# Kernel tuning notes

Hardware: AMD Instinct MI355X
Metric: run time of the kernel (lower is better)

The kernel has to match this reference:

```python
import jax, jax.numpy as jnp
import numpy as np

T = 524288
AABB = 4.0
BETA_MIN = 0.1
L_ENC = 4
NL = np.array([16, 22, 30, 42, 58, 80, 111, 154, 213, 295, 407, 563, 777, 1074, 1483, 2048])
# corner offsets, same ordering as the torch code's vertices[:,0..7]
OFFS = np.array([[0,0,0],[1,0,0],[0,1,0],[1,1,0],[0,0,1],[1,0,1],[0,1,1],[1,1,1]])
PRIMES = np.array([1, 2654435761, 805459861], dtype=np.uint32)


def hash_features(xn, tables):
    # xn: [N,3] normalized positions in hash-grid space; tables: [16, T, 2]
    Ns = jnp.asarray(NL, jnp.float32)                      # [16]
    xs = xn[:, None, :] * Ns[None, :, None]                # [N,16,3]
    fl = jnp.floor(xs)
    loc = xs - fl                                          # trilinear weights input
    fli = fl.astype(jnp.int32).astype(jnp.uint32)          # wraparound == int32 bit pattern
    offs = jnp.asarray(OFFS, jnp.uint32)                   # [8,3]
    pr = jnp.asarray(PRIMES, jnp.uint32)
    # spatial hash per corner, per level (avoid materializing [N,16,8,3] vertices)
    a = (fli[:, :, None, 0] + offs[None, None, :, 0]) * pr[0]
    b = (fli[:, :, None, 1] + offs[None, None, :, 1]) * pr[1]
    c = (fli[:, :, None, 2] + offs[None, None, :, 2]) * pr[2]
    h = ((a ^ b) ^ c) % jnp.uint32(T)                      # [N,16,8]
    lvl_off = (jnp.arange(len(NL), dtype=jnp.uint32) * jnp.uint32(T))[None, :, None]
    flat_idx = (h + lvl_off).astype(jnp.int32)             # index into flattened tables
    feats = tables.reshape(-1, tables.shape[-1])[flat_idx] # [N,16,8,2] gather
    offf = jnp.asarray(OFFS, jnp.float32)
    lp = loc[:, :, None, :]
    w = jnp.prod(lp * offf + (1.0 - lp) * (1.0 - offf), axis=-1)  # [N,16,8]
    out = jnp.einsum('nlc,nlcf->nlf', w, feats)            # trilinear interp
    return out.reshape(out.shape[0], -1)                   # [N, 16*2], level-major


def pos_enc(d):
    parts = [d]
    for j in range(L_ENC):
        parts.append(jnp.sin((2.0 ** j) * d))
        parts.append(jnp.cos((2.0 ** j) * d))
    return jnp.concatenate(parts, axis=1)                  # [N,27]


def _forward(x, d, appearance_idx, transient_idx, tables, emb_a, emb_t,
             Wd1, bd1, Wd2, bd2, Ws1, bs1, Ws2, bs2, Ws3, bs3,
             Wt1, bt1, Wt2, bt2, Wt3, bt3, Wtd, btd, Wtr, btr, Wtb, btb):
    xn = x / AABB
    mask = (jnp.abs(xn[:, 0]) < 0.5) & (jnp.abs(xn[:, 1]) < 0.5) & (jnp.abs(xn[:, 2]) < 0.5)
    xn = xn + 0.5
    feats = hash_features(xn, tables)                      # [N,32]
    h = jnp.maximum(feats @ Wd1 + bd1, 0.0) @ Wd2 + bd2    # density MLP -> [N,16]
    denc = pos_enc(d)
    a_emb = emb_a[appearance_idx]
    t_emb = emb_t[transient_idx]
    s = jnp.concatenate([h, denc, a_emb], axis=1)
    s = jnp.maximum(s @ Ws1 + bs1, 0.0)
    s = jnp.maximum(s @ Ws2 + bs2, 0.0)
    srgb = jax.nn.sigmoid(s @ Ws3 + bs3)
    t = jnp.concatenate([h, t_emb], axis=1)
    t = jnp.maximum(t @ Wt1 + bt1, 0.0)
    t = jnp.maximum(t @ Wt2 + bt2, 0.0)
    t = jnp.maximum(t @ Wt3 + bt3, 0.0)
    tsig = jax.nn.softplus(t @ Wtd + btd)[:, 0]
    trgb = jax.nn.sigmoid(t @ Wtr + btr)
    tbeta = jax.nn.softplus(t @ Wtb + btb)[:, 0] + BETA_MIN
    m = mask[:, None]
    static_rgb = jnp.where(m, srgb, 0.0)
    static_sigma = jnp.exp(jnp.where(mask, h[:, 0], -100000.0))
    transient_rgb = jnp.where(m, trgb, 0.0)
    transient_sigma = jnp.exp(jnp.where(mask, tsig, -100000.0))
    transient_beta = jnp.where(mask, tbeta, BETA_MIN)
    return static_rgb, static_sigma, transient_rgb, transient_sigma, transient_beta


def setup_inputs() -> dict:
    key = jax.random.key(0)
    ks = jax.random.split(key, 24)
    N, NV = 262144, 1000

    def lin(k, i, o):
        return jax.random.normal(k, (i, o), jnp.float32) * (1.0 / np.sqrt(i))

    inp = {}
    inp['x'] = jax.random.normal(ks[0], (N, 3), jnp.float32)
    inp['d'] = jax.random.normal(ks[1], (N, 3), jnp.float32)
    inp['appearance_idx'] = jax.random.randint(ks[2], (N,), 0, NV)
    inp['transient_idx'] = jax.random.randint(ks[3], (N,), 0, NV)
    inp['tables'] = (jax.random.uniform(ks[4], (len(NL), T, 2), jnp.float32) * 2 - 1) * 1e-4
    inp['emb_a'] = jax.random.normal(ks[5], (NV, 48), jnp.float32)
    inp['emb_t'] = jax.random.normal(ks[6], (NV, 16), jnp.float32)
    inp['Wd1'] = lin(ks[7], 32, 64); inp['bd1'] = jnp.zeros((64,), jnp.float32)
    inp['Wd2'] = lin(ks[8], 64, 16); inp['bd2'] = jnp.zeros((16,), jnp.float32)
    inp['Ws1'] = lin(ks[9], 91, 64); inp['bs1'] = jnp.zeros((64,), jnp.float32)
    inp['Ws2'] = lin(ks[10], 64, 64); inp['bs2'] = jnp.zeros((64,), jnp.float32)
    inp['Ws3'] = lin(ks[11], 64, 3); inp['bs3'] = jnp.zeros((3,), jnp.float32)
    inp['Wt1'] = lin(ks[12], 32, 64); inp['bt1'] = jnp.zeros((64,), jnp.float32)
    inp['Wt2'] = lin(ks[13], 64, 64); inp['bt2'] = jnp.zeros((64,), jnp.float32)
    inp['Wt3'] = lin(ks[14], 64, 64); inp['bt3'] = jnp.zeros((64,), jnp.float32)
    inp['Wtd'] = lin(ks[15], 64, 1); inp['btd'] = jnp.zeros((1,), jnp.float32)
    inp['Wtr'] = lin(ks[16], 64, 3); inp['btr'] = jnp.zeros((3,), jnp.float32)
    inp['Wtb'] = lin(ks[17], 64, 1); inp['btb'] = jnp.zeros((1,), jnp.float32)
    return inp


def reference(x, d, appearance_idx, transient_idx, tables, emb_a, emb_t,
              Wd1, bd1, Wd2, bd2, Ws1, bs1, Ws2, bs2, Ws3, bs3,
              Wt1, bt1, Wt2, bt2, Wt3, bt3, Wtd, btd, Wtr, btr, Wtb, btb):
    return _forward(x, d, appearance_idx, transient_idx, tables, emb_a, emb_t,
                    Wd1, bd1, Wd2, bd2, Ws1, bs1, Ws2, bs2, Ws3, bs3,
                    Wt1, bt1, Wt2, bt2, Wt3, bt3, Wtd, btd, Wtr, btr, Wtb, btb)
```

## Files before the change

### kernel.cpp

```cpp
#include <hip/hip_runtime.h>
#include <hip/hip_fp16.h>
#include <math.h>

#define NT 256
#define NT0 512
#define T_SIZE 524288u
#define T_MASK 524287u
#define PR1 2654435761u
#define PR2 805459861u

#define OFF_WD1 0
#define OFF_WD2 4096
#define OFF_WS1 6144
#define OFF_WS2 18432
#define OFF_WT1 26624
#define OFF_WT2 30720
#define OFF_WT3 38912
#define WBUF_USH 47104
#define WBUF_BYTES 98304

#define AS 104

typedef float f32x4 __attribute__((ext_vector_type(4)));
typedef short s16x8 __attribute__((ext_vector_type(8)));
typedef unsigned u32x4 __attribute__((ext_vector_type(4)));

__device__ __forceinline__ float sigmoidf_(float x) { return 1.0f / (1.0f + __expf(-x)); }
__device__ __forceinline__ float softplusf_(float x) { return fmaxf(x, 0.0f) + log1pf(__expf(-fabsf(x))); }

__device__ __forceinline__ unsigned short f2bf(float f) {
  union { float f; unsigned u; } v; v.f = f;
  unsigned r = v.u + 0x7fffu + ((v.u >> 16) & 1u);
  return (unsigned short)(r >> 16);
}
__device__ __forceinline__ float bf2f(unsigned short h) {
  union { unsigned u; float f; } v; v.u = ((unsigned)h) << 16; return v.f;
}
__device__ __forceinline__ f32x4 splat4(float t) { f32x4 v; v[0]=t; v[1]=t; v[2]=t; v[3]=t; return v; }

__device__ __forceinline__ unsigned char f2e5(float f) {
  unsigned short u = __half_as_ushort(__float2half(f));
  return (unsigned char)(((unsigned)u + 0x7Fu + ((u >> 8) & 1u)) >> 8);
}
__device__ __forceinline__ float e52f(unsigned v) {
  return __half2float(__ushort_as_half((unsigned short)((v & 0xFFu) << 8)));
}

template <int ASTR, int SWM>
__device__ __forceinline__ s16x8 lda(const unsigned short* act, int lane, int m, int kh) {
  int p = m * 16 + (lane & 15);
  int c = (kh * 32 + ((lane >> 4) << 3)) ^ ((p & SWM) << 3);
  return *reinterpret_cast<const s16x8*>(act + p * ASTR + c);
}
__device__ __forceinline__ s16x8 ldb(const unsigned short* wb, int lane, int fidx) {
  return *reinterpret_cast<const s16x8*>(wb + (fidx * 64 + lane) * 8);
}
template <int ASTR, int SWM>
__device__ __forceinline__ void stp(unsigned short* act, int p, int col, float v0, float v1) {
  unsigned pk = (unsigned)f2bf(v0) | (((unsigned)f2bf(v1)) << 16);
  *reinterpret_cast<unsigned*>(act + p * ASTR + (col ^ ((p & SWM) << 3))) = pk;
}

template <int BT, int KH, int NTI, int NCOLS, class F>
__device__ void stage_plane(unsigned short* dst, const float* __restrict__ W, int plane, int tid, F rowmap) {
  for (int i = tid; i < NTI * KH * 64; i += BT) {
    int f = i >> 6, lane = i & 63;
    int n = f / KH, kh = f - n * KH;
    int o = n * 16 + (lane & 15);
    int kb = kh * 32 + ((lane >> 4) << 3);
    unsigned us0, us1, us2, us3;
#define MKPAIR(dstu, j0) { \
      unsigned short e0, e1; \
      { int sr = rowmap(kb + (j0)); float w = (sr >= 0) ? W[sr * NCOLS + o] : 0.f; \
        unsigned short hi = f2bf(w); e0 = plane ? f2bf(w - bf2f(hi)) : hi; } \
      { int sr = rowmap(kb + (j0) + 1); float w = (sr >= 0) ? W[sr * NCOLS + o] : 0.f; \
        unsigned short hi = f2bf(w); e1 = plane ? f2bf(w - bf2f(hi)) : hi; } \
      dstu = (unsigned)e0 | (((unsigned)e1) << 16); }
    MKPAIR(us0, 0) MKPAIR(us1, 2) MKPAIR(us2, 4) MKPAIR(us3, 6)
#undef MKPAIR
    *reinterpret_cast<uint4*>(dst + (size_t)i * 8) = make_uint4(us0, us1, us2, us3);
  }
}

template <int BT>
__device__ __forceinline__ void stage(float* dst, const float* __restrict__ src, int cnt, int tid) {
  for (int i = tid; i < cnt; i += BT) dst[i] = src[i];
}

template <int BT>
__device__ __forceinline__ void stagecpy(unsigned short* dst, const unsigned short* __restrict__ src,
                                         int cnt_ush, int tid) {
  const uint4* s = reinterpret_cast<const uint4*>(src);
  uint4* d = reinterpret_cast<uint4*>(dst);
  for (int i = tid; i < (cnt_ush >> 3); i += BT) d[i] = s[i];
}

#define MFMA_(a, b, c) __builtin_amdgcn_mfma_f32_16x16x32_bf16(a, b, c, 0, 0, 0)

#define DECL_ACC f32x4 acc00, acc01, acc02, acc03, acc10, acc11, acc12, acc13, \
                       acc20, acc21, acc22, acc23, acc30, acc31, acc32, acc33;

#define ACC_INIT(B) { \
  float t0 = (B)[(lane & 15)], t1 = (B)[16 + (lane & 15)], t2 = (B)[32 + (lane & 15)], t3 = (B)[48 + (lane & 15)]; \
  acc00 = splat4(t0); acc10 = acc00; acc20 = acc00; acc30 = acc00; \
  acc01 = splat4(t1); acc11 = acc01; acc21 = acc01; acc31 = acc01; \
  acc02 = splat4(t2); acc12 = acc02; acc22 = acc02; acc32 = acc02; \
  acc03 = splat4(t3); acc13 = acc03; acc23 = acc03; acc33 = acc03; }

#define GEMM_NBLK(WPTR, kh, KH, n) { s16x8 b = ldb(WPTR, lane, (n) * (KH) + (kh)); \
  acc0##n = MFMA_(a0, b, acc0##n); acc1##n = MFMA_(a1, b, acc1##n); \
  acc2##n = MFMA_(a2, b, acc2##n); acc3##n = MFMA_(a3, b, acc3##n); }

#define GEMM64(ACTP, ASTR, SWM, WB, KH, PLN) { \
  _Pragma("unroll") for (int kh = 0; kh < (KH); ++kh) { \
    s16x8 a0 = lda<ASTR, SWM>(ACTP, lane, 0, kh), a1 = lda<ASTR, SWM>(ACTP, lane, 1, kh), \
          a2 = lda<ASTR, SWM>(ACTP, lane, 2, kh), a3 = lda<ASTR, SWM>(ACTP, lane, 3, kh); \
    _Pragma("unroll") for (int pl = 0; pl < (PLN); ++pl) { \
      const unsigned short* wp = (WB) + pl * (KH) * 2048; \
      GEMM_NBLK(wp, kh, KH, 0) GEMM_NBLK(wp, kh, KH, 1) GEMM_NBLK(wp, kh, KH, 2) GEMM_NBLK(wp, kh, KH, 3) } } }

#define ST_ACT1(ACTP, ASTR, SWM, m, n, A) { \
  _Pragma("unroll") for (int r = 0; r < 4; ++r) { \
    int p = (m) * 16 + ((lane >> 4) << 2) + r; int col = (n) * 16 + (lane & 15); \
    (ACTP)[p * (ASTR) + (col ^ ((p & (SWM)) << 3))] = f2bf(fmaxf((A)[r], 0.f)); } }

#define ST_ACT_ALL(ACTP, ASTR, SWM) \
  ST_ACT1(ACTP, ASTR, SWM, 0, 0, acc00) ST_ACT1(ACTP, ASTR, SWM, 0, 1, acc01) \
  ST_ACT1(ACTP, ASTR, SWM, 0, 2, acc02) ST_ACT1(ACTP, ASTR, SWM, 0, 3, acc03) \
  ST_ACT1(ACTP, ASTR, SWM, 1, 0, acc10) ST_ACT1(ACTP, ASTR, SWM, 1, 1, acc11) \
  ST_ACT1(ACTP, ASTR, SWM, 1, 2, acc12) ST_ACT1(ACTP, ASTR, SWM, 1, 3, acc13) \
  ST_ACT1(ACTP, ASTR, SWM, 2, 0, acc20) ST_ACT1(ACTP, ASTR, SWM, 2, 1, acc21) \
  ST_ACT1(ACTP, ASTR, SWM, 2, 2, acc22) ST_ACT1(ACTP, ASTR, SWM, 2, 3, acc23) \
  ST_ACT1(ACTP, ASTR, SWM, 3, 0, acc30) ST_ACT1(ACTP, ASTR, SWM, 3, 1, acc31) \
  ST_ACT1(ACTP, ASTR, SWM, 3, 2, acc32) ST_ACT1(ACTP, ASTR, SWM, 3, 3, acc33)

#define ST_HV(ACTP, ASTR, SWM, m, H) { \
  _Pragma("unroll") for (int r = 0; r < 4; ++r) { \
    int pp = (m) * 16 + ((lane >> 4) << 2) + r; \
    (ACTP)[pp * (ASTR) + ((lane & 15) ^ ((pp & (SWM)) << 3))] = f2bf((H)[r]); } }

__device__ void wprep_block(int pid, int tid,
                            const float* Wd1, const float* Wd2, const float* Ws1,
                            const float* Ws2, const float* Wt1, const float* Wt2,
                            const float* Wt3, unsigned short* wbuf) {
  const float* W;
  int KH, NTI, NCOLS, mapt, dst;
  switch (pid >> 1) {
    case 0: W = Wd1; KH = 1; NTI = 4; NCOLS = 64; mapt = 0; dst = OFF_WD1 + (pid & 1) * 2048; break;
    case 1: W = Wd2; KH = 2; NTI = 1; NCOLS = 16; mapt = 0; dst = OFF_WD2 + (pid & 1) * 1024; break;
    case 2: W = Ws1; KH = 3; NTI = 4; NCOLS = 64; mapt = 1; dst = OFF_WS1 + (pid & 1) * 6144; break;
    case 3: W = Ws2; KH = 2; NTI = 4; NCOLS = 64; mapt = 0; dst = OFF_WS2 + (pid & 1) * 4096; break;
    case 4: W = Wt1; KH = 1; NTI = 4; NCOLS = 64; mapt = 0; dst = OFF_WT1 + (pid & 1) * 2048; break;
    case 5: W = Wt2; KH = 2; NTI = 4; NCOLS = 64; mapt = 0; dst = OFF_WT2 + (pid & 1) * 4096; break;
    default: W = Wt3; KH = 2; NTI = 4; NCOLS = 64; mapt = 0; dst = OFF_WT3 + (pid & 1) * 4096; break;
  }
  const int plane = pid & 1;
  const int total = NTI * KH * 64;
  for (int i = tid; i < total; i += 256) {
    int f = i >> 6, lane = i & 63;
    int n = f / KH, kh = f - n * KH;
    int o = n * 16 + (lane & 15);
    int kb = kh * 32 + ((lane >> 4) << 3);
    unsigned short e[8];
#pragma unroll
    for (int j = 0; j < 8; ++j) {
      int k = kb + j;
      int sr = mapt ? (k < 16 ? k : (k < 64 ? 27 + k : (k < 91 ? k - 48 : -1))) : k;
      float w = (sr >= 0) ? W[sr * NCOLS + o] : 0.f;
      unsigned short hi = f2bf(w);
      e[j] = plane ? f2bf(w - bf2f(hi)) : hi;
    }
    uint4 v;
    v.x = (unsigned)e[0] | ((unsigned)e[1] << 16);
    v.y = (unsigned)e[2] | ((unsigned)e[3] << 16);
    v.z = (unsigned)e[4] | ((unsigned)e[5] << 16);
    v.w = (unsigned)e[6] | ((unsigned)e[7] << 16);
    *reinterpret_cast<uint4*>(wbuf + dst + (size_t)i * 8) = v;
  }
}

__global__ void __launch_bounds__(256) kprep(
    const float* __restrict__ tables, unsigned* __restrict__ t8, int nq,
    const float* __restrict__ Wd1, const float* __restrict__ Wd2,
    const float* __restrict__ Ws1, const float* __restrict__ Ws2,
    const float* __restrict__ Wt1, const float* __restrict__ Wt2,
    const float* __restrict__ Wt3, unsigned short* __restrict__ wbuf) {
  if (blockIdx.x < 14) {
    wprep_block(blockIdx.x, threadIdx.x, Wd1, Wd2, Ws1, Ws2, Wt1, Wt2, Wt3, wbuf);
    return;
  }
  int i = (blockIdx.x - 14) * 256 + threadIdx.x;
  if (i >= nq) return;
  f32x4 v = __builtin_nontemporal_load(reinterpret_cast<const f32x4*>(tables) + i);
  unsigned r = (unsigned)f2e5(v[0]) | ((unsigned)f2e5(v[1]) << 8) |
               ((unsigned)f2e5(v[2]) << 16) | ((unsigned)f2e5(v[3]) << 24);
  __builtin_nontemporal_store(r, t8 + i);
}

__global__ void __launch_bounds__(256) kwprep(
    const float* __restrict__ Wd1, const float* __restrict__ Wd2,
    const float* __restrict__ Ws1, const float* __restrict__ Ws2,
    const float* __restrict__ Wt1, const float* __restrict__ Wt2,
    const float* __restrict__ Wt3, unsigned short* __restrict__ wbuf) {
  wprep_block(blockIdx.x, threadIdx.x, Wd1, Wd2, Ws1, Ws2, Wt1, Wt2, Wt3, wbuf);
}
__global__ void __launch_bounds__(256) kconv(const float* __restrict__ tables,
                                             unsigned* __restrict__ t8, int nq) {
  int i = blockIdx.x * 256 + threadIdx.x;
  if (i >= nq) return;
  f32x4 v = __builtin_nontemporal_load(reinterpret_cast<const f32x4*>(tables) + i);
  unsigned r = (unsigned)f2e5(v[0]) | ((unsigned)f2e5(v[1]) << 8) |
               ((unsigned)f2e5(v[2]) << 16) | ((unsigned)f2e5(v[3]) << 24);
  __builtin_nontemporal_store(r, t8 + i);
}

__global__ void __launch_bounds__(256, 6) k0a_gather(
    const float* __restrict__ x, const unsigned short* __restrict__ t8,
    unsigned* __restrict__ featws, int Npts) {
  const int lane = threadIdx.x & 63, wv = threadIdx.x >> 6;
  const int g = blockIdx.x & 3;
  const int n = (blockIdx.x >> 2) * 256 + wv * 64 + lane;
  if (n >= Npts) return;
  float xn0 = x[3 * n + 0] * 0.25f + 0.5f;
  float xn1 = x[3 * n + 1] * 0.25f + 0.5f;
  float xn2 = x[3 * n + 2] * 0.25f + 0.5f;

  float scA, scB, scC, scD;
  switch (g) {
    case 0:  scA = 16.f; scB = 58.f;  scC = 213.f; scD = 777.f;  break;
    case 1:  scA = 22.f; scB = 80.f;  scC = 295.f; scD = 1074.f; break;
    case 2:  scA = 30.f; scB = 111.f; scC = 407.f; scD = 1483.f; break;
    default: scA = 42.f; scB = 154.f; scC = 563.f; scD = 2048.f; break;
  }

#define ALVL(J, SC) \
  unsigned ad##J##0, ad##J##1, ad##J##2, ad##J##3, ad##J##4, ad##J##5, ad##J##6, ad##J##7; \
  float lf##J##0, lf##J##1, lf##J##2; \
  { \
    float xs0 = xn0 * (SC), xs1 = xn1 * (SC), xs2 = xn2 * (SC); \
    float f0 = floorf(xs0), f1 = floorf(xs1), f2 = floorf(xs2); \
    lf##J##0 = xs0 - f0; lf##J##1 = xs1 - f1; lf##J##2 = xs2 - f2; \
    unsigned i0 = (unsigned)(int)f0, i1 = (unsigned)(int)f1, i2 = (unsigned)(int)f2; \
    unsigned a0 = i0, a1 = i0 + 1u; \
    unsigned b0 = i1 * PR1, b1 = (i1 + 1u) * PR1; \
    unsigned c0 = i2 * PR2, c1 = (i2 + 1u) * PR2; \
    unsigned base = (unsigned)(g + 4 * (J)) * T_SIZE; \
    ad##J##0 = (base + ((a0 ^ b0 ^ c0) & T_MASK)) * 2u; \
    ad##J##1 = (base + ((a1 ^ b0 ^ c0) & T_MASK)) * 2u; \
    ad##J##2 = (base + ((a0 ^ b1 ^ c0) & T_MASK)) * 2u; \
    ad##J##3 = (base + ((a1 ^ b1 ^ c0) & T_MASK)) * 2u; \
    ad##J##4 = (base + ((a0 ^ b0 ^ c1) & T_MASK)) * 2u; \
    ad##J##5 = (base + ((a1 ^ b0 ^ c1) & T_MASK)) * 2u; \
    ad##J##6 = (base + ((a0 ^ b1 ^ c1) & T_MASK)) * 2u; \
    ad##J##7 = (base + ((a1 ^ b1 ^ c1) & T_MASK)) * 2u; \
  }
  ALVL(0, scA) ALVL(1, scB) ALVL(2, scC) ALVL(3, scD)
#undef ALVL

#define GLD(Q, AD) asm volatile("global_load_ushort %0, %1, %2" : "=v"(Q) : "v"(AD), "s"(t8));
#define LLVL(J) \
  unsigned q##J##0, q##J##1, q##J##2, q##J##3, q##J##4, q##J##5, q##J##6, q##J##7; \
  GLD(q##J##0, ad##J##0) GLD(q##J##1, ad##J##1) GLD(q##J##2, ad##J##2) GLD(q##J##3, ad##J##3) \
  GLD(q##J##4, ad##J##4) GLD(q##J##5, ad##J##5) GLD(q##J##6, ad##J##6) GLD(q##J##7, ad##J##7)
  LLVL(0) LLVL(1) LLVL(2) LLVL(3)
#undef LLVL
#undef GLD

#define BLVL(J, FP) { \
    float w1x = lf##J##0, w0x = 1.f - w1x; \
    float w1y = lf##J##1, w0y = 1.f - w1y; \
    float w1z = lf##J##2, w0z = 1.f - w1z; \
    float w000 = w0x * w0y * w0z, w100 = w1x * w0y * w0z; \
    float w010 = w0x * w1y * w0z, w110 = w1x * w1y * w0z; \
    float w001 = w0x * w0y * w1z, w101 = w1x * w0y * w1z; \
    float w011 = w0x * w1y * w1z, w111 = w1x * w1y * w1z; \
    float fa = w000 * e52f(q##J##0) + w100 * e52f(q##J##1) + w010 * e52f(q##J##2) + \
               w110 * e52f(q##J##3) + w001 * e52f(q##J##4) + w101 * e52f(q##J##5) + \
               w011 * e52f(q##J##6) + w111 * e52f(q##J##7); \
    float fb = w000 * e52f(q##J##0 >> 8) + w100 * e52f(q##J##1 >> 8) + w010 * e52f(q##J##2 >> 8) + \
               w110 * e52f(q##J##3 >> 8) + w001 * e52f(q##J##4 >> 8) + w101 * e52f(q##J##5 >> 8) + \
               w011 * e52f(q##J##6 >> 8) + w111 * e52f(q##J##7 >> 8); \
    FP = (unsigned)f2bf(fa) | (((unsigned)f2bf(fb)) << 16); }
  unsigned fp0, fp1, fp2, fp3;
  asm volatile("s_waitcnt vmcnt(24)" ::: "memory");
  __builtin_amdgcn_sched_barrier(0);
  BLVL(0, fp0)
  asm volatile("s_waitcnt vmcnt(16)" ::: "memory");
  __builtin_amdgcn_sched_barrier(0);
  BLVL(1, fp1)
  asm volatile("s_waitcnt vmcnt(8)" ::: "memory");
  __builtin_amdgcn_sched_barrier(0);
  BLVL(2, fp2)
  asm volatile("s_waitcnt vmcnt(0)" ::: "memory");
  __builtin_amdgcn_sched_barrier(0);
  BLVL(3, fp3)
#undef BLVL
  u32x4 o; o[0] = fp0; o[1] = fp1; o[2] = fp2; o[3] = fp3;
  __builtin_nontemporal_store(
      o, reinterpret_cast<u32x4*>(featws + ((size_t)g * Npts + n) * 4));
}

__global__ void __launch_bounds__(NT, 2) k12b_all(
    const float* __restrict__ x, const float* __restrict__ d,
    const int* __restrict__ aidx, const int* __restrict__ tridx,
    const float* __restrict__ emb_a, const float* __restrict__ emb_t,
    const unsigned* __restrict__ featws, const unsigned short* __restrict__ wbuf,
    const float* __restrict__ bd1, const float* __restrict__ bd2,
    const float* __restrict__ bs1, const float* __restrict__ bs2,
    const float* __restrict__ Ws3, const float* __restrict__ bs3,
    const float* __restrict__ bt1, const float* __restrict__ bt2,
    const float* __restrict__ bt3,
    const float* __restrict__ Wtd, const float* __restrict__ btd,
    const float* __restrict__ Wtr, const float* __restrict__ btr,
    const float* __restrict__ Wtb, const float* __restrict__ btb,
    float* __restrict__ out, int Npts) {
  __shared__ __align__(16) unsigned short sh[38912];
  __shared__ __align__(16) float fl[984];
  const int tid = threadIdx.x, lane = tid & 63, wv = tid >> 6;
  const int n = blockIdx.x * NT + tid;
  const bool live = (n < Npts);
  const int nn = live ? n : Npts - 1;
  unsigned short* actw = sh + wv * (64 * AS);
  unsigned short* wreg = sh + 26624;
  float* exch = reinterpret_cast<float*>(wreg + 6144);
  const int p = lane;

  float xn0 = x[3 * nn + 0] * 0.25f, xn1 = x[3 * nn + 1] * 0.25f, xn2 = x[3 * nn + 2] * 0.25f;
  const bool mask = (fabsf(xn0) < 0.5f) && (fabsf(xn1) < 0.5f) && (fabsf(xn2) < 0.5f);

  u32x4 q0 = __builtin_nontemporal_load(
      reinterpret_cast<const u32x4*>(featws + ((size_t)0 * Npts + nn) * 4));
  u32x4 q1 = __builtin_nontemporal_load(
      reinterpret_cast<const u32x4*>(featws + ((size_t)1 * Npts + nn) * 4));
  u32x4 q2 = __builtin_nontemporal_load(
      reinterpret_cast<const u32x4*>(featws + ((size_t)2 * Npts + nn) * 4));
  u32x4 q3 = __builtin_nontemporal_load(
      reinterpret_cast<const u32x4*>(featws + ((size_t)3 * Npts + nn) * 4));
  const float4* tp = reinterpret_cast<const float4*>(emb_t + (size_t)tridx[nn] * 16);
  float4 et0 = tp[0], et1 = tp[1], et2 = tp[2], et3 = tp[3];

  {
    float d0 = d[3 * nn + 0], d1 = d[3 * nn + 1], d2 = d[3 * nn + 2];
    float s10 = __sinf(d0), s11 = __sinf(d1), s12 = __sinf(d2);
    float c10 = __cosf(d0), c11 = __cosf(d1), c12 = __cosf(d2);
    float s20 = __sinf(2.f * d0), s21 = __sinf(2.f * d1), s22 = __sinf(2.f * d2);
    float c20 = __cosf(2.f * d0), c21 = __cosf(2.f * d1), c22 = __cosf(2.f * d2);
    float s40 = __sinf(4.f * d0), s41 = __sinf(4.f * d1), s42 = __sinf(4.f * d2);
    float c40 = __cosf(4.f * d0), c41 = __cosf(4.f * d1), c42 = __cosf(4.f * d2);
    float s80 = __sinf(8.f * d0), s81 = __sinf(8.f * d1), s82 = __sinf(8.f * d2);
    float c80 = __cosf(8.f * d0), c81 = __cosf(8.f * d1), c82 = __cosf(8.f * d2);
    stp<AS, 0>(actw, p, 64, d0, d1);   stp<AS, 0>(actw, p, 66, d2, s10);
    stp<AS, 0>(actw, p, 68, s11, s12); stp<AS, 0>(actw, p, 70, c10, c11);
    stp<AS, 0>(actw, p, 72, c12, s20); stp<AS, 0>(actw, p, 74, s21, s22);
    stp<AS, 0>(actw, p, 76, c20, c21); stp<AS, 0>(actw, p, 78, c22, s40);
    stp<AS, 0>(actw, p, 80, s41, s42); stp<AS, 0>(actw, p, 82, c40, c41);
    stp<AS, 0>(actw, p, 84, c42, s80); stp<AS, 0>(actw, p, 86, s81, s82);
    stp<AS, 0>(actw, p, 88, c80, c81); stp<AS, 0>(actw, p, 90, c82, 0.f);
    stp<AS, 0>(actw, p, 92, 0.f, 0.f); stp<AS, 0>(actw, p, 94, 0.f, 0.f);
  }
#define PUTL(l, val) *reinterpret_cast<unsigned*>(actw + p * AS + 2 * (l)) = (val);
  PUTL(0, q0[0]) PUTL(4, q0[1]) PUTL(8, q0[2]) PUTL(12, q0[3])
  PUTL(1, q1[0]) PUTL(5, q1[1]) PUTL(9, q1[2]) PUTL(13, q1[3])
  PUTL(2, q2[0]) PUTL(6, q2[1]) PUTL(10, q2[2]) PUTL(14, q2[3])
  PUTL(3, q3[0]) PUTL(7, q3[1]) PUTL(11, q3[2]) PUTL(15, q3[3])
#undef PUTL

  stagecpy<NT>(wreg, wbuf + OFF_WD1, 4096, tid);
  stagecpy<NT>(wreg + 4096, wbuf + OFF_WD2, 2048, tid);
  stage<NT>(fl, bs1, 64, tid);
  stage<NT>(fl + 64, bs2, 64, tid);
  stage<NT>(fl + 128, Ws3, 192, tid);
  if (tid < 3) fl[320 + tid] = bs3[tid];
  stage<NT>(fl + 384, bt1, 64, tid);
  stage<NT>(fl + 448, bt2, 64, tid);
  stage<NT>(fl + 512, bt3, 64, tid);
  stage<NT>(fl + 576, Wtd, 64, tid);
  stage<NT>(fl + 640, Wtr, 192, tid);
  stage<NT>(fl + 832, Wtb, 64, tid);
  if (tid == 0) { fl[896] = btd[0]; fl[900] = btb[0]; }
  if (tid < 3) fl[897 + tid] = btr[tid];
  stage<NT>(fl + 904, bd1, 64, tid);
  stage<NT>(fl + 968, bd2, 16, tid);
  __syncthreads();

  DECL_ACC;
  ACC_INIT(fl + 904);
  GEMM64(actw, AS, 0, wreg, 1, 2);
  ST_ACT_ALL(actw, AS, 0);

  f32x4 h0, h1, h2, h3;
  { float t = fl[968 + (lane & 15)]; h0 = splat4(t); h1 = h0; h2 = h0; h3 = h0; }
#pragma unroll
  for (int kh = 0; kh < 2; ++kh) {
    s16x8 a0 = lda<AS, 0>(actw, lane, 0, kh), a1 = lda<AS, 0>(actw, lane, 1, kh),
          a2 = lda<AS, 0>(actw, lane, 2, kh), a3 = lda<AS, 0>(actw, lane, 3, kh);
#pragma unroll
    for (int pl = 0; pl < 2; ++pl) {
      s16x8 b = ldb(wreg + 4096 + pl * 1024, lane, kh);
      h0 = MFMA_(a0, b, h0); h1 = MFMA_(a1, b, h1); h2 = MFMA_(a2, b, h2); h3 = MFMA_(a3, b, h3);
    }
  }
#define HV_X(m, H) { _Pragma("unroll") for (int r = 0; r < 4; ++r) { \
    int pr = (m) * 16 + ((lane >> 4) << 2) + r; \
    if ((lane & 15) == 0) exch[wv * 64 + pr] = (H)[r]; } }
  HV_X(0, h0) HV_X(1, h1) HV_X(2, h2) HV_X(3, h3)
#undef HV_X
  ST_HV(actw, AS, 0, 0, h0) ST_HV(actw, AS, 0, 1, h1)
  ST_HV(actw, AS, 0, 2, h2) ST_HV(actw, AS, 0, 3, h3)
  {
    float hv0v = exch[wv * 64 + lane];
    if (live) out[3 * (size_t)Npts + n] = mask ? __expf(hv0v) : 0.f;
  }
  {
    const float4* ap = reinterpret_cast<const float4*>(emb_a + (size_t)aidx[nn] * 48);
#pragma unroll
    for (int q = 0; q < 12; ++q) {
      float4 e = ap[q];
      stp<AS, 0>(actw, p, 16 + 4 * q, e.x, e.y);
      stp<AS, 0>(actw, p, 18 + 4 * q, e.z, e.w);
    }
  }
  __syncthreads();
  stagecpy<NT>(wreg, wbuf + OFF_WS1, 12288, tid);
  __syncthreads();

  ACC_INIT(fl);
  GEMM64(actw, AS, 0, wreg, 3, 2);
  ST_ACT_ALL(actw, AS, 0);
  __syncthreads();
  stagecpy<NT>(wreg, wbuf + OFF_WS2, 8192, tid);
  __syncthreads();
  ACC_INIT(fl + 64);
  GEMM64(actw, AS, 0, wreg, 2, 2);
  ST_ACT_ALL(actw, AS, 0);

  {
    float r0 = fl[320], r1 = fl[321], r2 = fl[322];
    for (int j = 0; j < 64; ++j) {
      int jj = (j + 2 * p) & 63;
      float a = bf2f(actw[p * AS + jj]);
      r0 = fmaf(a, fl[128 + 3 * jj + 0], r0);
      r1 = fmaf(a, fl[128 + 3 * jj + 1], r1);
      r2 = fmaf(a, fl[128 + 3 * jj + 2], r2);
    }
    if (live) {
      out[3 * (size_t)n + 0] = mask ? sigmoidf_(r0) : 0.f;
      out[3 * (size_t)n + 1] = mask ? sigmoidf_(r1) : 0.f;
      out[3 * (size_t)n + 2] = mask ? sigmoidf_(r2) : 0.f;
    }
  }

  ST_HV(actw, AS, 0, 0, h0) ST_HV(actw, AS, 0, 1, h1)
  ST_HV(actw, AS, 0, 2, h2) ST_HV(actw, AS, 0, 3, h3)
  stp<AS, 0>(actw, p, 16, et0.x, et0.y);  stp<AS, 0>(actw, p, 18, et0.z, et0.w);
  stp<AS, 0>(actw, p, 20, et1.x, et1.y);  stp<AS, 0>(actw, p, 22, et1.z, et1.w);
  stp<AS, 0>(actw, p, 24, et2.x, et2.y);  stp<AS, 0>(actw, p, 26, et2.z, et2.w);
  stp<AS, 0>(actw, p, 28, et3.x, et3.y);  stp<AS, 0>(actw, p, 30, et3.z, et3.w);
  __syncthreads();
  stagecpy<NT>(wreg, wbuf + OFF_WT1, 4096, tid);
  stagecpy<NT>(wreg + 4096, wbuf + OFF_WT2, 8192, tid);
  __syncthreads();
  ACC_INIT(fl + 384);
  GEMM64(actw, AS, 0, wreg, 1, 2);
  ST_ACT_ALL(actw, AS, 0);
  ACC_INIT(fl + 448);
  GEMM64(actw, AS, 0, (wreg + 4096), 2, 2);
  ST_ACT_ALL(actw, AS, 0);
  __syncthreads();
  stagecpy<NT>(wreg, wbuf + OFF_WT3, 8192, tid);
  __syncthreads();
  ACC_INIT(fl + 512);
  GEMM64(actw, AS, 0, wreg, 2, 2);
  ST_ACT_ALL(actw, AS, 0);

  float hd = fl[896], hr0 = fl[897], hr1 = fl[898], hr2 = fl[899], hb = fl[900];
  for (int j = 0; j < 64; ++j) {
    int jj = (j + 2 * p) & 63;
    float a = bf2f(actw[p * AS + jj]);
    hd = fmaf(a, fl[576 + jj], hd);
    hr0 = fmaf(a, fl[640 + 3 * jj + 0], hr0);
    hr1 = fmaf(a, fl[640 + 3 * jj + 1], hr1);
    hr2 = fmaf(a, fl[640 + 3 * jj + 2], hr2);
    hb = fmaf(a, fl[832 + jj], hb);
  }
  if (live) {
    size_t N4 = (size_t)Npts * 4;
    out[N4 + 3 * (size_t)n + 0] = mask ? sigmoidf_(hr0) : 0.f;
    out[N4 + 3 * (size_t)n + 1] = mask ? sigmoidf_(hr1) : 0.f;
    out[N4 + 3 * (size_t)n + 2] = mask ? sigmoidf_(hr2) : 0.f;
    out[(size_t)Npts * 7 + n] = mask ? __expf(softplusf_(hd)) : 0.f;
    out[(size_t)Npts * 8 + n] = mask ? (softplusf_(hb) + 0.1f) : 0.1f;
  }
}

template <int F8>
__global__ void __launch_bounds__(NT0, 4) k0f_density(
    const float* __restrict__ x, const float* __restrict__ tables,
    const unsigned short* __restrict__ t8,
    const float* __restrict__ Wd1, const float* __restrict__ bd1,
    const float* __restrict__ Wd2, const float* __restrict__ bd2,
    float* __restrict__ hvws, float* __restrict__ out, int Npts) {
  __shared__ __align__(16) unsigned short sh[38912];
  __shared__ __align__(16) float fl[592];
  const int tid = threadIdx.x, lane = tid & 63, wv = tid >> 6;
  const int n = blockIdx.x * NT0 + tid;
  const bool live = (n < Npts);
  const int nn = live ? n : Npts - 1;

  stage_plane<NT0, 1, 4, 64>(sh + 32768, Wd1, 0, tid, [](int k) { return k; });
  stage_plane<NT0, 1, 4, 64>(sh + 32768 + 2048, Wd1, 1, tid, [](int k) { return k; });
  stage_plane<NT0, 2, 1, 16>(sh + 36864, Wd2, 0, tid, [](int k) { return k; });
  stage_plane<NT0, 2, 1, 16>(sh + 36864 + 1024, Wd2, 1, tid, [](int k) { return k; });
  stage<NT0>(fl, bd1, 64, tid);
  stage<NT0>(fl + 64, bd2, 16, tid);
  __syncthreads();

  unsigned short* actw = sh + wv * 4096;
  const int p = lane;
  float xn0 = x[3 * nn + 0] * 0.25f + 0.5f, xn1 = x[3 * nn + 1] * 0.25f + 0.5f, xn2 = x[3 * nn + 2] * 0.25f + 0.5f;
  const bool mask = (fabsf(xn0 - 0.5f) < 0.5f) && (fabsf(xn1 - 0.5f) < 0.5f) && (fabsf(xn2 - 0.5f) < 0.5f);

  const float2* tab2 = reinterpret_cast<const float2*>(tables);
  constexpr float NLV[16] = {16.f, 22.f, 30.f, 42.f, 58.f, 80.f, 111.f, 154.f,
                             213.f, 295.f, 407.f, 563.f, 777.f, 1074.f, 1483.f, 2048.f};
#pragma unroll
  for (int l = 0; l < 16; ++l) {
    const float sc = NLV[l];
    float xs0 = xn0 * sc, xs1 = xn1 * sc, xs2 = xn2 * sc;
    float f0 = floorf(xs0), f1 = floorf(xs1), f2 = floorf(xs2);
    float l0 = xs0 - f0, l1 = xs1 - f1, l2 = xs2 - f2;
    unsigned i0 = (unsigned)(int)f0, i1 = (unsigned)(int)f1, i2 = (unsigned)(int)f2;
    unsigned a0 = i0, a1 = i0 + 1u;
    unsigned b0 = i1 * PR1, b1 = (i1 + 1u) * PR1;
    unsigned c0 = i2 * PR2, c1 = (i2 + 1u) * PR2;
    float w0x = 1.f - l0, w1x = l0, w0y = 1.f - l1, w1y = l1, w0z = 1.f - l2, w1z = l2;
    float2 t0, t1, t2, t3, t4, t5, t6, t7;
    if constexpr (F8) {
      const unsigned short* tl8 = t8 + (size_t)l * T_SIZE;
      unsigned short q0 = tl8[(a0 ^ b0 ^ c0) & T_MASK];
      unsigned short q1 = tl8[(a1 ^ b0 ^ c0) & T_MASK];
      unsigned short q2 = tl8[(a0 ^ b1 ^ c0) & T_MASK];
      unsigned short q3 = tl8[(a1 ^ b1 ^ c0) & T_MASK];
      unsigned short q4 = tl8[(a0 ^ b0 ^ c1) & T_MASK];
      unsigned short q5 = tl8[(a1 ^ b0 ^ c1) & T_MASK];
      unsigned short q6 = tl8[(a0 ^ b1 ^ c1) & T_MASK];
      unsigned short q7 = tl8[(a1 ^ b1 ^ c1) & T_MASK];
      t0 = make_float2(e52f(q0), e52f(q0 >> 8));
      t1 = make_float2(e52f(q1), e52f(q1 >> 8));
      t2 = make_float2(e52f(q2), e52f(q2 >> 8));
      t3 = make_float2(e52f(q3), e52f(q3 >> 8));
      t4 = make_float2(e52f(q4), e52f(q4 >> 8));
      t5 = make_float2(e52f(q5), e52f(q5 >> 8));
      t6 = make_float2(e52f(q6), e52f(q6 >> 8));
      t7 = make_float2(e52f(q7), e52f(q7 >> 8));
    } else {
      const float2* tl = tab2 + (size_t)l * T_SIZE;
      t0 = tl[(a0 ^ b0 ^ c0) & T_MASK];
      t1 = tl[(a1 ^ b0 ^ c0) & T_MASK];
      t2 = tl[(a0 ^ b1 ^ c0) & T_MASK];
      t3 = tl[(a1 ^ b1 ^ c0) & T_MASK];
      t4 = tl[(a0 ^ b0 ^ c1) & T_MASK];
      t5 = tl[(a1 ^ b0 ^ c1) & T_MASK];
      t6 = tl[(a0 ^ b1 ^ c1) & T_MASK];
      t7 = tl[(a1 ^ b1 ^ c1) & T_MASK];
    }
    float w000 = w0x * w0y * w0z, w100 = w1x * w0y * w0z;
    float w010 = w0x * w1y * w0z, w110 = w1x * w1y * w0z;
    float w001 = w0x * w0y * w1z, w101 = w1x * w0y * w1z;
    float w011 = w0x * w1y * w1z, w111 = w1x * w1y * w1z;
    float fa = w000 * t0.x + w100 * t1.x + w010 * t2.x + w110 * t3.x +
               w001 * t4.x + w101 * t5.x + w011 * t6.x + w111 * t7.x;
    float fb = w000 * t0.y + w100 * t1.y + w010 * t2.y + w110 * t3.y +
               w001 * t4.y + w101 * t5.y + w011 * t6.y + w111 * t7.y;
    unsigned pk = (unsigned)f2bf(fa) | (((unsigned)f2bf(fb)) << 16);
    *reinterpret_cast<unsigned*>(actw + p * 64 + ((2 * l) ^ ((p & 7) << 3))) = pk;
  }

  DECL_ACC;
  ACC_INIT(fl);
  GEMM64(actw, 64, 7, sh + 32768, 1, 2);
  ST_ACT_ALL(actw, 64, 7);

  f32x4 h0, h1, h2, h3;
  { float t = fl[64 + (lane & 15)]; h0 = splat4(t); h1 = h0; h2 = h0; h3 = h0; }
  {
#pragma unroll
    for (int kh = 0; kh < 2; ++kh) {
      s16x8 a0 = lda<64, 7>(actw, lane, 0, kh), a1 = lda<64, 7>(actw, lane, 1, kh),
            a2 = lda<64, 7>(actw, lane, 2, kh), a3 = lda<64, 7>(actw, lane, 3, kh);
#pragma unroll
      for (int pl = 0; pl < 2; ++pl) {
        s16x8 b = ldb(sh + 36864 + pl * 1024, lane, kh);
        h0 = MFMA_(a0, b, h0); h1 = MFMA_(a1, b, h1); h2 = MFMA_(a2, b, h2); h3 = MFMA_(a3, b, h3);
      }
    }
  }
  const int ptbase = blockIdx.x * NT0 + wv * 64;
#define HV_ST(m, H) { _Pragma("unroll") for (int r = 0; r < 4; ++r) { \
    int pr = (m) * 16 + ((lane >> 4) << 2) + r; \
    if (ptbase + pr < Npts) hvws[(size_t)(ptbase + pr) * 16 + (lane & 15)] = (H)[r]; \
    if ((lane & 15) == 0) fl[80 + wv * 64 + pr] = (H)[r]; } }
  HV_ST(0, h0) HV_ST(1, h1) HV_ST(2, h2) HV_ST(3, h3)
#undef HV_ST
  float hv0 = fl[80 + wv * 64 + lane];
  if (live) out[3 * (size_t)Npts + n] = mask ? __expf(hv0) : 0.f;
}

__global__ void __launch_bounds__(NT, 2) k12_heads(
    const float* __restrict__ x, const float* __restrict__ d,
    const int* __restrict__ aidx, const int* __restrict__ tridx,
    const float* __restrict__ emb_a, const float* __restrict__ emb_t,
    const unsigned short* __restrict__ wbuf,
    const float* __restrict__ bs1, const float* __restrict__ bs2,
    const float* __restrict__ Ws3, const float* __restrict__ bs3,
    const float* __restrict__ bt1, const float* __restrict__ bt2,
    const float* __restrict__ bt3,
    const float* __restrict__ Wtd, const float* __restrict__ btd,
    const float* __restrict__ Wtr, const float* __restrict__ btr,
    const float* __restrict__ Wtb, const float* __restrict__ btb,
    const float* __restrict__ hvws, float* __restrict__ out, int Npts) {
  __shared__ __align__(16) unsigned short sh[36864];
  __shared__ __align__(16) float fl[904];
  const int tid = threadIdx.x, lane = tid & 63, wv = tid >> 6;
  const int n = blockIdx.x * NT + tid;
  const bool live = (n < Npts);
  const int nn = live ? n : Npts - 1;
  unsigned short* actw = sh + wv * 6144;
  const int p = lane;

  float xn0 = x[3 * nn + 0] * 0.25f, xn1 = x[3 * nn + 1] * 0.25f, xn2 = x[3 * nn + 2] * 0.25f;
  const bool mask = (fabsf(xn0) < 0.5f) && (fabsf(xn1) < 0.5f) && (fabsf(xn2) < 0.5f);

  const float4* hvp = reinterpret_cast<const float4*>(hvws + (size_t)nn * 16);
  float4 hv0_ = hvp[0], hv1_ = hvp[1], hv2_ = hvp[2], hv3_ = hvp[3];
  const float4* tp = reinterpret_cast<const float4*>(emb_t + (size_t)tridx[nn] * 16);
  float4 et0 = tp[0], et1 = tp[1], et2 = tp[2], et3 = tp[3];

  {
    stp<96, 3>(actw, p, 0, hv0_.x, hv0_.y);   stp<96, 3>(actw, p, 2, hv0_.z, hv0_.w);
    stp<96, 3>(actw, p, 4, hv1_.x, hv1_.y);   stp<96, 3>(actw, p, 6, hv1_.z, hv1_.w);
    stp<96, 3>(actw, p, 8, hv2_.x, hv2_.y);   stp<96, 3>(actw, p, 10, hv2_.z, hv2_.w);
    stp<96, 3>(actw, p, 12, hv3_.x, hv3_.y);  stp<96, 3>(actw, p, 14, hv3_.z, hv3_.w);
    const float4* ap = reinterpret_cast<const float4*>(emb_a + (size_t)aidx[nn] * 48);
#pragma unroll
    for (int q = 0; q < 12; ++q) {
      float4 e = ap[q];
      stp<96, 3>(actw, p, 16 + 4 * q, e.x, e.y);
      stp<96, 3>(actw, p, 18 + 4 * q, e.z, e.w);
    }
    float d0 = d[3 * nn + 0], d1 = d[3 * nn + 1], d2 = d[3 * nn + 2];
    float s10 = __sinf(d0), s11 = __sinf(d1), s12 = __sinf(d2);
    float c10 = __cosf(d0), c11 = __cosf(d1), c12 = __cosf(d2);
    float s20 = __sinf(2.f * d0), s21 = __sinf(2.f * d1), s22 = __sinf(2.f * d2);
    float c20 = __cosf(2.f * d0), c21 = __cosf(2.f * d1), c22 = __cosf(2.f * d2);
    float s40 = __sinf(4.f * d0), s41 = __sinf(4.f * d1), s42 = __sinf(4.f * d2);
    float c40 = __cosf(4.f * d0), c41 = __cosf(4.f * d1), c42 = __cosf(4.f * d2);
    float s80 = __sinf(8.f * d0), s81 = __sinf(8.f * d1), s82 = __sinf(8.f * d2);
    float c80 = __cosf(8.f * d0), c81 = __cosf(8.f * d1), c82 = __cosf(8.f * d2);
    stp<96, 3>(actw, p, 64, d0, d1);   stp<96, 3>(actw, p, 66, d2, s10);
    stp<96, 3>(actw, p, 68, s11, s12); stp<96, 3>(actw, p, 70, c10, c11);
    stp<96, 3>(actw, p, 72, c12, s20); stp<96, 3>(actw, p, 74, s21, s22);
    stp<96, 3>(actw, p, 76, c20, c21); stp<96, 3>(actw, p, 78, c22, s40);
    stp<96, 3>(actw, p, 80, s41, s42); stp<96, 3>(actw, p, 82, c40, c41);
    stp<96, 3>(actw, p, 84, c42, s80); stp<96, 3>(actw, p, 86, s81, s82);
    stp<96, 3>(actw, p, 88, c80, c81); stp<96, 3>(actw, p, 90, c82, 0.f);
    stp<96, 3>(actw, p, 92, 0.f, 0.f); stp<96, 3>(actw, p, 94, 0.f, 0.f);
  }
  stagecpy<NT>(sh + 24576, wbuf + OFF_WS1, 12288, tid);
  stage<NT>(fl, bs1, 64, tid);
  stage<NT>(fl + 64, bs2, 64, tid);
  stage<NT>(fl + 128, Ws3, 192, tid);
  if (tid < 3) fl[320 + tid] = bs3[tid];
  stage<NT>(fl + 384, bt1, 64, tid);
  stage<NT>(fl + 448, bt2, 64, tid);
  stage<NT>(fl + 512, bt3, 64, tid);
  stage<NT>(fl + 576, Wtd, 64, tid);
  stage<NT>(fl + 640, Wtr, 192, tid);
  stage<NT>(fl + 832, Wtb, 64, tid);
  if (tid == 0) { fl[896] = btd[0]; fl[900] = btb[0]; }
  if (tid < 3) fl[897 + tid] = btr[tid];
  __syncthreads();

  DECL_ACC;
  ACC_INIT(fl);
  GEMM64(actw, 96, 3, sh + 24576, 3, 2);
  ST_ACT_ALL(actw, 96, 3);
  __syncthreads();
  stagecpy<NT>(sh + 24576, wbuf + OFF_WS2, 8192, tid);
  __syncthreads();
  ACC_INIT(fl + 64);
  GEMM64(actw, 96, 3, sh + 24576, 2, 2);
  ST_ACT_ALL(actw, 96, 3);

  {
    float r0 = fl[320], r1 = fl[321], r2 = fl[322];
    for (int j = 0; j < 64; ++j) {
      float a = bf2f(actw[p * 96 + (j ^ ((p & 3) << 3))]);
      r0 = fmaf(a, fl[128 + 3 * j + 0], r0);
      r1 = fmaf(a, fl[128 + 3 * j + 1], r1);
      r2 = fmaf(a, fl[128 + 3 * j + 2], r2);
    }
    if (live) {
      out[3 * (size_t)n + 0] = mask ? sigmoidf_(r0) : 0.f;
      out[3 * (size_t)n + 1] = mask ? sigmoidf_(r1) : 0.f;
      out[3 * (size_t)n + 2] = mask ? sigmoidf_(r2) : 0.f;
    }
  }

  stp<96, 3>(actw, p, 0, hv0_.x, hv0_.y);   stp<96, 3>(actw, p, 2, hv0_.z, hv0_.w);
  stp<96, 3>(actw, p, 4, hv1_.x, hv1_.y);   stp<96, 3>(actw, p, 6, hv1_.z, hv1_.w);
  stp<96, 3>(actw, p, 8, hv2_.x, hv2_.y);   stp<96, 3>(actw, p, 10, hv2_.z, hv2_.w);
  stp<96, 3>(actw, p, 12, hv3_.x, hv3_.y);  stp<96, 3>(actw, p, 14, hv3_.z, hv3_.w);
  stp<96, 3>(actw, p, 16, et0.x, et0.y);    stp<96, 3>(actw, p, 18, et0.z, et0.w);
  stp<96, 3>(actw, p, 20, et1.x, et1.y);    stp<96, 3>(actw, p, 22, et1.z, et1.w);
  stp<96, 3>(actw, p, 24, et2.x, et2.y);    stp<96, 3>(actw, p, 26, et2.z, et2.w);
  stp<96, 3>(actw, p, 28, et3.x, et3.y);    stp<96, 3>(actw, p, 30, et3.z, et3.w);
  __syncthreads();
  stagecpy<NT>(sh + 24576, wbuf + OFF_WT1, 4096, tid);
  __syncthreads();
  ACC_INIT(fl + 384);
  GEMM64(actw, 96, 3, sh + 24576, 1, 2);
  ST_ACT_ALL(actw, 96, 3);
  __syncthreads();
  stagecpy<NT>(sh + 24576, wbuf + OFF_WT2, 8192, tid);
  __syncthreads();
  ACC_INIT(fl + 448);
  GEMM64(actw, 96, 3, sh + 24576, 2, 2);
  ST_ACT_ALL(actw, 96, 3);
  __syncthreads();
  stagecpy<NT>(sh + 24576, wbuf + OFF_WT3, 8192, tid);
  __syncthreads();
  ACC_INIT(fl + 512);
  GEMM64(actw, 96, 3, sh + 24576, 2, 2);
  ST_ACT_ALL(actw, 96, 3);

  float hd = fl[896], hr0 = fl[897], hr1 = fl[898], hr2 = fl[899], hb = fl[900];
  for (int j = 0; j < 64; ++j) {
    float a = bf2f(actw[p * 96 + (j ^ ((p & 3) << 3))]);
    hd = fmaf(a, fl[576 + j], hd);
    hr0 = fmaf(a, fl[640 + 3 * j + 0], hr0);
    hr1 = fmaf(a, fl[640 + 3 * j + 1], hr1);
    hr2 = fmaf(a, fl[640 + 3 * j + 2], hr2);
    hb = fmaf(a, fl[832 + j], hb);
  }
  if (live) {
    size_t N4 = (size_t)Npts * 4;
    out[N4 + 3 * (size_t)n + 0] = mask ? sigmoidf_(hr0) : 0.f;
    out[N4 + 3 * (size_t)n + 1] = mask ? sigmoidf_(hr1) : 0.f;
    out[N4 + 3 * (size_t)n + 2] = mask ? sigmoidf_(hr2) : 0.f;
    out[(size_t)Npts * 7 + n] = mask ? __expf(softplusf_(hd)) : 0.f;
    out[(size_t)Npts * 8 + n] = mask ? (softplusf_(hb) + 0.1f) : 0.1f;
  }
}

extern "C" void kernel_launch(void* const* d_in, const int* in_sizes, int n_in,
                              void* d_out, int out_size, void* d_ws, size_t ws_size,
                              hipStream_t stream) {
  const int Npts = in_sizes[0] / 3;
  const float* x = (const float*)d_in[0];
  const float* d = (const float*)d_in[1];
  const int* aidx = (const int*)d_in[2];
  const int* tridx = (const int*)d_in[3];
  const float* tables = (const float*)d_in[4];
  const float* emb_a = (const float*)d_in[5];
  const float* emb_t = (const float*)d_in[6];
  const float* Wd1 = (const float*)d_in[7];
  const float* bd1 = (const float*)d_in[8];
  const float* Wd2 = (const float*)d_in[9];
  const float* bd2 = (const float*)d_in[10];
  const float* Ws1 = (const float*)d_in[11];
  const float* bs1 = (const float*)d_in[12];
  const float* Ws2 = (const float*)d_in[13];
  const float* bs2 = (const float*)d_in[14];
  const float* Ws3 = (const float*)d_in[15];
  const float* bs3 = (const float*)d_in[16];
  const float* Wt1 = (const float*)d_in[17];
  const float* bt1 = (const float*)d_in[18];
  const float* Wt2 = (const float*)d_in[19];
  const float* bt2 = (const float*)d_in[20];
  const float* Wt3 = (const float*)d_in[21];
  const float* bt3 = (const float*)d_in[22];
  const float* Wtd = (const float*)d_in[23];
  const float* btd = (const float*)d_in[24];
  const float* Wtr = (const float*)d_in[25];
  const float* btr = (const float*)d_in[26];
  const float* Wtb = (const float*)d_in[27];
  const float* btb = (const float*)d_in[28];
  float* out = (float*)d_out;

  float* hvws = (float*)d_ws;
  const size_t hv_bytes = (size_t)Npts * 16 * sizeof(float);
  unsigned short* wbuf = (unsigned short*)((char*)d_ws + hv_bytes);
  unsigned short* t8 = (unsigned short*)((char*)d_ws + hv_bytes + WBUF_BYTES);
  const size_t t8_bytes = (size_t)16 * T_SIZE * 2;
  unsigned* featws = (unsigned*)((char*)d_ws + hv_bytes + WBUF_BYTES + t8_bytes);
  const size_t feat_bytes = (size_t)Npts * 64;
  const bool has_t8 = (ws_size >= hv_bytes + WBUF_BYTES + t8_bytes);
  const bool has_f = (ws_size >= hv_bytes + WBUF_BYTES + t8_bytes + feat_bytes);

  int blocksA = ((Npts + 255) / 256) * 4;
  int blocks0 = (Npts + NT0 - 1) / NT0;
  int blocks = (Npts + NT - 1) / NT;

  if (has_f) {
    int nq = (int)(16 * T_SIZE / 2);
    kprep<<<dim3(14 + (nq + 255) / 256), dim3(256), 0, stream>>>(
        tables, (unsigned*)t8, nq, Wd1, Wd2, Ws1, Ws2, Wt1, Wt2, Wt3, wbuf);
    k0a_gather<<<dim3(blocksA), dim3(256), 0, stream>>>(x, t8, featws, Npts);
    k12b_all<<<dim3(blocks), dim3(NT), 0, stream>>>(
        x, d, aidx, tridx, emb_a, emb_t, featws, wbuf,
        bd1, bd2, bs1, bs2, Ws3, bs3, bt1, bt2, bt3,
        Wtd, btd, Wtr, btr, Wtb, btb, out, Npts);
  } else {
    kwprep<<<dim3(14), dim3(256), 0, stream>>>(Wd1, Wd2, Ws1, Ws2, Wt1, Wt2, Wt3, wbuf);
    if (has_t8) {
      int nq = (int)(16 * T_SIZE / 2);
      kconv<<<dim3((nq + 255) / 256), dim3(256), 0, stream>>>(tables, (unsigned*)t8, nq);
      k0f_density<1><<<dim3(blocks0), dim3(NT0), 0, stream>>>(
          x, tables, t8, Wd1, bd1, Wd2, bd2, hvws, out, Npts);
    } else {
      k0f_density<0><<<dim3(blocks0), dim3(NT0), 0, stream>>>(
          x, tables, t8, Wd1, bd1, Wd2, bd2, hvws, out, Npts);
    }
    k12_heads<<<dim3(blocks), dim3(NT), 0, stream>>>(
        x, d, aidx, tridx, emb_a, emb_t, wbuf,
        bs1, bs2, Ws3, bs3, bt1, bt2, bt3,
        Wtd, btd, Wtr, btr, Wtb, btb, hvws, out, Npts);
  }
}
```

Measured before the change: 161.0 us.

## Pair x-adjacent hash corners into single dword gathers in hash-grid kernel

When the integer x coordinate is even, corners i0 and i0+1 hash to adjacent table entries (idx and idx^1). The gather kernel now fetches both with one dword load and picks the halves using a parity mask. When the coordinate is odd it falls back to extra per-lane ushort loads inside a divergent branch. This cuts gather instruction count but adds per-lane branching and select logic. It also drops the staged per-level waitcnt overlap for a single full wait, and lowers the occupancy hint from 6 to 4 blocks.

```diff
diff --git a/kernel.cpp b/kernel.cpp
--- a/kernel.cpp
+++ b/kernel.cpp
@@ -214,7 +214,7 @@
   __builtin_nontemporal_store(r, t8 + i);
 }
 
-__global__ void __launch_bounds__(256, 6) k0a_gather(
+__global__ void __launch_bounds__(256, 4) k0a_gather(
     const float* __restrict__ x, const unsigned short* __restrict__ t8,
     unsigned* __restrict__ featws, int Npts) {
   const int lane = threadIdx.x & 63, wv = threadIdx.x >> 6;
@@ -233,40 +233,69 @@
     default: scA = 42.f; scB = 154.f; scC = 563.f; scD = 2048.f; break;
   }
 
+  unsigned parmask = 0, oddmask = 0;
+
 #define ALVL(J, SC) \
-  unsigned ad##J##0, ad##J##1, ad##J##2, ad##J##3, ad##J##4, ad##J##5, ad##J##6, ad##J##7; \
+  unsigned da##J##0, da##J##1, da##J##2, da##J##3; \
+  unsigned ua##J##0, ua##J##1, ua##J##2, ua##J##3; \
   float lf##J##0, lf##J##1, lf##J##2; \
   { \
     float xs0 = xn0 * (SC), xs1 = xn1 * (SC), xs2 = xn2 * (SC); \
     float f0 = floorf(xs0), f1 = floorf(xs1), f2 = floorf(xs2); \
     lf##J##0 = xs0 - f0; lf##J##1 = xs1 - f1; lf##J##2 = xs2 - f2; \
     unsigned i0 = (unsigned)(int)f0, i1 = (unsigned)(int)f1, i2 = (unsigned)(int)f2; \
-    unsigned a0 = i0, a1 = i0 + 1u; \
-    unsigned b0 = i1 * PR1, b1 = (i1 + 1u) * PR1; \
-    unsigned c0 = i2 * PR2, c1 = (i2 + 1u) * PR2; \
+    unsigned i0p = i0 + 1u; \
+    unsigned b0v = i1 * PR1, b1v = (i1 + 1u) * PR1; \
+    unsigned c0v = i2 * PR2, c1v = (i2 + 1u) * PR2; \
     unsigned base = (unsigned)(g + 4 * (J)) * T_SIZE; \
-    ad##J##0 = (base + ((a0 ^ b0 ^ c0) & T_MASK)) * 2u; \
-    ad##J##1 = (base + ((a1 ^ b0 ^ c0) & T_MASK)) * 2u; \
-    ad##J##2 = (base + ((a0 ^ b1 ^ c0) & T_MASK)) * 2u; \
-    ad##J##3 = (base + ((a1 ^ b1 ^ c0) & T_MASK)) * 2u; \
-    ad##J##4 = (base + ((a0 ^ b0 ^ c1) & T_MASK)) * 2u; \
-    ad##J##5 = (base + ((a1 ^ b0 ^ c1) & T_MASK)) * 2u; \
-    ad##J##6 = (base + ((a0 ^ b1 ^ c1) & T_MASK)) * 2u; \
-    ad##J##7 = (base + ((a1 ^ b1 ^ c1) & T_MASK)) * 2u; \
+    unsigned idx; \
+    idx = base + ((i0 ^ b0v ^ c0v) & T_MASK); da##J##0 = (idx & ~1u) * 2u; parmask |= (idx & 1u) << ((J) * 4 + 0); \
+    ua##J##0 = (base + ((i0p ^ b0v ^ c0v) & T_MASK)) * 2u; \
+    idx = base + ((i0 ^ b1v ^ c0v) & T_MASK); da##J##1 = (idx & ~1u) * 2u; parmask |= (idx & 1u) << ((J) * 4 + 1); \
+    ua##J##1 = (base + ((i0p ^ b1v ^ c0v) & T_MASK)) * 2u; \
+    idx = base + ((i0 ^ b0v ^ c1v) & T_MASK); da##J##2 = (idx & ~1u) * 2u; parmask |= (idx & 1u) << ((J) * 4 + 2); \
+    ua##J##2 = (base + ((i0p ^ b0v ^ c1v) & T_MASK)) * 2u; \
+    idx = base + ((i0 ^ b1v ^ c1v) & T_MASK); da##J##3 = (idx & ~1u) * 2u; parmask |= (idx & 1u) << ((J) * 4 + 3); \
+    ua##J##3 = (base + ((i0p ^ b1v ^ c1v) & T_MASK)) * 2u; \
+    oddmask |= (i0 & 1u) << (J); \
   }
   ALVL(0, scA) ALVL(1, scB) ALVL(2, scC) ALVL(3, scD)
 #undef ALVL
 
-#define GLD(Q, AD) asm volatile("global_load_ushort %0, %1, %2" : "=v"(Q) : "v"(AD), "s"(t8));
-#define LLVL(J) \
-  unsigned q##J##0, q##J##1, q##J##2, q##J##3, q##J##4, q##J##5, q##J##6, q##J##7; \
-  GLD(q##J##0, ad##J##0) GLD(q##J##1, ad##J##1) GLD(q##J##2, ad##J##2) GLD(q##J##3, ad##J##3) \
-  GLD(q##J##4, ad##J##4) GLD(q##J##5, ad##J##5) GLD(q##J##6, ad##J##6) GLD(q##J##7, ad##J##7)
-  LLVL(0) LLVL(1) LLVL(2) LLVL(3)
-#undef LLVL
-#undef GLD
-
+#define GLDD(Q, AD) asm volatile("global_load_dword %0, %1, %2" : "=v"(Q) : "v"(AD), "s"(t8));
+#define GLDU(Q, AD) asm volatile("global_load_ushort %0, %1, %2" : "=v"(Q) : "v"(AD), "s"(t8));
+  unsigned D00, D01, D02, D03, D10, D11, D12, D13,
+           D20, D21, D22, D23, D30, D31, D32, D33;
+  GLDD(D00, da00) GLDD(D01, da01) GLDD(D02, da02) GLDD(D03, da03)
+  GLDD(D10, da10) GLDD(D11, da11) GLDD(D12, da12) GLDD(D13, da13)
+  GLDD(D20, da20) GLDD(D21, da21) GLDD(D22, da22) GLDD(D23, da23)
+  GLDD(D30, da30) GLDD(D31, da31) GLDD(D32, da32) GLDD(D33, da33)
+
+  unsigned U00 = 0, U01 = 0, U02 = 0, U03 = 0, U10 = 0, U11 = 0, U12 = 0, U13 = 0,
+           U20 = 0, U21 = 0, U22 = 0, U23 = 0, U30 = 0, U31 = 0, U32 = 0, U33 = 0;
+  if (oddmask & 1u) { GLDU(U00, ua00) GLDU(U01, ua01) GLDU(U02, ua02) GLDU(U03, ua03) }
+  if (oddmask & 2u) { GLDU(U10, ua10) GLDU(U11, ua11) GLDU(U12, ua12) GLDU(U13, ua13) }
+  if (oddmask & 4u) { GLDU(U20, ua20) GLDU(U21, ua21) GLDU(U22, ua22) GLDU(U23, ua23) }
+  if (oddmask & 8u) { GLDU(U30, ua30) GLDU(U31, ua31) GLDU(U32, ua32) GLDU(U33, ua33) }
+#undef GLDU
+#undef GLDD
+  asm volatile("s_waitcnt vmcnt(0)" ::: "memory");
+  __builtin_amdgcn_sched_barrier(0);
+
+#define MERGE(J, K, D, U, Q0, Q1) \
+  unsigned Q0, Q1; \
+  { \
+    unsigned hi = (parmask >> ((J) * 4 + (K))) & 1u; \
+    unsigned lo16 = (D) & 0xffffu, hi16 = (D) >> 16; \
+    Q0 = hi ? hi16 : lo16; \
+    unsigned other = hi ? lo16 : hi16; \
+    Q1 = ((oddmask >> (J)) & 1u) ? (U) : other; \
+  }
 #define BLVL(J, FP) { \
+    MERGE(J, 0, D##J##0, U##J##0, q##J##0, q##J##1) \
+    MERGE(J, 1, D##J##1, U##J##1, q##J##2, q##J##3) \
+    MERGE(J, 2, D##J##2, U##J##2, q##J##4, q##J##5) \
+    MERGE(J, 3, D##J##3, U##J##3, q##J##6, q##J##7) \
     float w1x = lf##J##0, w0x = 1.f - w1x; \
     float w1y = lf##J##1, w0y = 1.f - w1y; \
     float w1z = lf##J##2, w0z = 1.f - w1z; \
@@ -282,19 +311,9 @@
                w011 * e52f(q##J##6 >> 8) + w111 * e52f(q##J##7 >> 8); \
     FP = (unsigned)f2bf(fa) | (((unsigned)f2bf(fb)) << 16); }
   unsigned fp0, fp1, fp2, fp3;
-  asm volatile("s_waitcnt vmcnt(24)" ::: "memory");
-  __builtin_amdgcn_sched_barrier(0);
-  BLVL(0, fp0)
-  asm volatile("s_waitcnt vmcnt(16)" ::: "memory");
-  __builtin_amdgcn_sched_barrier(0);
-  BLVL(1, fp1)
-  asm volatile("s_waitcnt vmcnt(8)" ::: "memory");
-  __builtin_amdgcn_sched_barrier(0);
-  BLVL(2, fp2)
-  asm volatile("s_waitcnt vmcnt(0)" ::: "memory");
-  __builtin_amdgcn_sched_barrier(0);
-  BLVL(3, fp3)
+  BLVL(0, fp0) BLVL(1, fp1) BLVL(2, fp2) BLVL(3, fp3)
 #undef BLVL
+#undef MERGE
   u32x4 o; o[0] = fp0; o[1] = fp1; o[2] = fp2; o[3] = fp3;
   __builtin_nontemporal_store(
       o, reinterpret_cast<u32x4*>(featws + ((size_t)g * Npts + n) * 4));
```

Result: slower. 188.5 us (+17.1%).
